# Kernel optimization log

Hardware: AMD Instinct MI355X
Metric: run time of the kernel (lower is better)

The kernel has to match this reference:

```python
import jax, jax.numpy as jnp
import numpy as np

B, S, N, E = 8, 32, 512, 8192
RC = DC = 64; SC = 256; EC = 512; P = 12


def setup_inputs() -> dict:
    key = jax.random.key(0)
    ks = jax.random.split(key, 20)
    def rn(k, shape, s=0.05):
        return jax.random.normal(k, shape, jnp.float32) * s
    return {
        "x": jax.random.normal(ks[0], (B, S, N), jnp.float32),
        "edge_index": jax.random.randint(ks[1], (2, E), 0, N),
        "edge_weight": jax.random.uniform(ks[2], (E,), jnp.float32),
        "start_w": rn(ks[3], (RC, 1)), "start_b": rn(ks[4], (RC,)),
        "filt_w": rn(ks[5], (DC, RC, 2)), "filt_b": rn(ks[6], (DC,)),
        "gate_w": rn(ks[7], (DC, RC, 2)), "gate_b": rn(ks[8], (DC,)),
        "gcn_w": rn(ks[9], (DC, DC)), "gcn_b": rn(ks[10], (DC,)),
        "res_w": rn(ks[11], (RC, DC)), "res_b": rn(ks[12], (RC,)),
        "skip_w": rn(ks[13], (SC, DC)), "skip_b": rn(ks[14], (SC,)),
        "end1_w": rn(ks[15], (EC, SC)), "end1_b": rn(ks[16], (EC,)),
        "end2_w": rn(ks[17], (P, EC)), "end2_b": rn(ks[18], (P,)),
    }


def _conv1x1(x, w, b):
    # Conv2d kernel (1,1): pure channel mix. x: [B,C,N,T], w: [O,C]
    return jnp.einsum('bcnt,oc->bont', x, w) + b[None, :, None, None]


def _conv_time2(x, w, b):
    return (jnp.einsum('bcnt,oc->bont', x[..., :-1], w[..., 0])
            + jnp.einsum('bcnt,oc->bont', x[..., 1:], w[..., 1])
            + b[None, :, None, None])


def _gcn_adj(edge_index, edge_weight, n):
    # PyG gcn_norm: add self-loops (weight 1), symmetric D^-1/2 (A+I) D^-1/2,
    # aggregation at edge_index[1] (target). Returns dense A_hat[tgt, src].
    ar = jnp.arange(n)
    row = jnp.concatenate([edge_index[0], ar])
    col = jnp.concatenate([edge_index[1], ar])
    w = jnp.concatenate([edge_weight, jnp.ones((n,), edge_weight.dtype)])
    deg = jnp.zeros((n,), w.dtype).at[col].add(w)
    dis = jnp.where(deg > 0, jax.lax.rsqrt(deg), jnp.zeros_like(deg))
    norm = dis[row] * w * dis[col]
    return jnp.zeros((n, n), w.dtype).at[col, row].add(norm)


def reference(x, edge_index, edge_weight, start_w, start_b, filt_w, filt_b,
              gate_w, gate_b, gcn_w, gcn_b, res_w, res_b, skip_w, skip_b,
              end1_w, end1_b, end2_w, end2_b):
    n = x.shape[2]
    A = _gcn_adj(edge_index, edge_weight, n)           # [N,N] sparse->dense (N small)
    h = jnp.transpose(x, (0, 2, 1))[:, None]           # [B,1,N,T]
    h = _conv1x1(h, start_w, start_b)                  # [B,RC,N,T]
    residual = h
    f = _conv_time2(h, filt_w, filt_b)                 # [B,DC,N,T-1]
    g = _conv_time2(h, gate_w, gate_b)
    # GCNConv applied to every (batch, time) slice == batched graph matmul
    fg = jnp.einsum('bcnt,oc->bont', f, gcn_w)         # x @ W^T
    fg = jnp.einsum('mn,bont->bomt', A, fg) + gcn_b[None, :, None, None]
    hg = jnp.tanh(fg) * jax.nn.sigmoid(g)              # gated activation
    skip = _conv1x1(hg, skip_w, skip_b)                # [B,SC,N,T-1]
    h = _conv1x1(hg, res_w, res_b) + residual[..., -hg.shape[3]:]
    out = jax.nn.relu(skip)
    out = jax.nn.relu(_conv1x1(out, end1_w, end1_b))
    out = _conv1x1(out, end2_w, end2_b)                # [B,P,N,T-1]
    # adaptive_avg_pool2d((N,1)) with H already N -> mean over time, squeeze
    return out.mean(axis=3)                            # [B,P,N]
```

## Files before the change

kernel.cpp:

```cpp
#include <hip/hip_runtime.h>

#define B_ 8
#define S_ 32
#define N_ 512
#define E_ 8192
#define T_ 31

typedef __attribute__((ext_vector_type(8))) __bf16 bf16x8;
typedef __attribute__((ext_vector_type(4))) float f32x4;
typedef unsigned short u16;
typedef unsigned int u32;

__device__ __forceinline__ u16 f2b(float f) {
    union { float f; u32 u; } v; v.f = f;
    u32 r = v.u + 0x7FFF + ((v.u >> 16) & 1);
    return (u16)(r >> 16);
}

__device__ __forceinline__ u32 cvtpk(float lo, float hi) {
    u32 r;
    asm("v_cvt_pk_bf16_f32 %0, %1, %2" : "=v"(r) : "v"(lo), "v"(hi));
    return r;
}

__device__ __forceinline__ f32x4 mfma16(bf16x8 a, bf16x8 b, f32x4 c) {
    return __builtin_amdgcn_mfma_f32_16x16x32_bf16(a, b, c, 0, 0, 0);
}

__global__ void deg_k(const int* __restrict__ ei, const float* __restrict__ ew,
                      float* __restrict__ deg) {
    int e = blockIdx.x * 256 + threadIdx.x;
    if (e >= E_ + N_) return;
    int col; float w;
    if (e < E_) { col = ei[E_ + e]; w = ew[e]; }
    else        { col = e - E_;     w = 1.f;  }
    atomicAdd(deg + col, w);
}

__global__ void dis_coef_k(const float* __restrict__ deg, float* __restrict__ dis,
                           const float* __restrict__ start_w, const float* __restrict__ start_b,
                           const float* __restrict__ filt_w, const float* __restrict__ filt_b,
                           const float* __restrict__ gate_w, const float* __restrict__ gate_b,
                           const float* __restrict__ gcn_w, float* __restrict__ coef,
                           const float* __restrict__ end2_b, float* __restrict__ out) {
    if (blockIdx.x >= 3) {
        int i = (blockIdx.x - 3) * 256 + threadIdx.x;
        out[i] = end2_b[(i >> 9) % 12];
        return;
    }
    if (blockIdx.x < 2) {
        int n = blockIdx.x * 256 + threadIdx.x;
        float d = deg[n];
        dis[n] = (d > 0.f) ? rsqrtf(d) : 0.f;
        return;
    }
    __shared__ float W[16384];
    __shared__ float sw[64], sb[64], A0[64], A1[64], C0[64];
    const int tid = threadIdx.x;
    if (tid < 64) { sw[tid] = start_w[tid]; sb[tid] = start_b[tid]; }
#pragma unroll
    for (int k = 0; k < 32; ++k) W[tid + k * 256] = filt_w[tid + k * 256];
#pragma unroll
    for (int k = 0; k < 32; ++k) W[8192 + tid + k * 256] = gate_w[tid + k * 256];
    __syncthreads();
    if (tid < 128) {
        const int o = tid & 63;
        const float* Wb = W + ((tid >= 64) ? 8192 : 0);
        float a0 = 0, a1 = 0, c = 0;
        for (int rr = 0; rr < 64; ++rr) {
            int r = (rr + o) & 63;
            float f0 = Wb[(o * 64 + r) * 2], f1 = Wb[(o * 64 + r) * 2 + 1];
            a0 += f0 * sw[r]; a1 += f1 * sw[r]; c += (f0 + f1) * sb[r];
        }
        if (tid < 64) { A0[o] = a0; A1[o] = a1; C0[o] = c + filt_b[o]; }
        else { coef[192 + o] = a0; coef[256 + o] = a1; coef[320 + o] = c + gate_b[o]; }
    }
    __syncthreads();
#pragma unroll
    for (int k = 0; k < 16; ++k) W[tid + k * 256] = gcn_w[tid + k * 256];
    __syncthreads();
    if (tid < 64) {
        const int o = tid;
        float u0 = 0, u1 = 0, u2 = 0;
        for (int dd = 0; dd < 64; ++dd) {
            int d = (dd + o) & 63;
            float g = W[o * 64 + d];
            u0 += g * A0[d]; u1 += g * A1[d]; u2 += g * C0[d];
        }
        coef[o] = u0; coef[64 + o] = u1; coef[128 + o] = u2;
    }
}

__global__ void scat_wconv_k(const int* __restrict__ ei, const float* __restrict__ ew,
                             const float* __restrict__ dis,
                             const float* __restrict__ skip_w, const float* __restrict__ end1_w,
                             const float* __restrict__ end2_w,
                             u16* __restrict__ W1, u16* __restrict__ W2, u16* __restrict__ W3,
                             float* __restrict__ S, float* __restrict__ rs) {
    const int bid = blockIdx.x;
    if (bid < 512) {
        int i = bid * 256 + threadIdx.x;
        {
            int m = i & 7, lane = (i >> 3) & 63, ii = (i >> 9) & 3;
            int kkI = (i >> 11) & 7, pw = (i >> 14) & 1, wid = (i >> 15) & 3;
            int er = wid * 128 + pw * 64 + ii * 16 + (lane & 15);
            int col = kkI * 32 + (lane >> 4) * 8 + m;
            W2[i] = f2b(end1_w[er * 256 + col]);
        }
        if (i < 16384) {
            int m = i & 7, lane = (i >> 3) & 63, ii = (i >> 9) & 3;
            int kkI = (i >> 11) & 1, wid = (i >> 12) & 3;
            int sr = wid * 64 + ii * 16 + (lane & 15);
            int col = kkI * 32 + (lane >> 4) * 8 + m;
            W1[i] = f2b(skip_w[sr * 64 + col]);
        }
        if (i < 8192) {
            int m = i & 7, lane = (i >> 3) & 63, c = (i >> 9) & 1;
            int pw = (i >> 10) & 1, wid = (i >> 11) & 3;
            int p = lane & 15;
            int k = wid * 128 + pw * 64 + c * 32 + (lane >> 4) * 8 + m;
            int e = (k & 0x1E0) | (((k >> 3) & 3) << 2) | (k & 3) | (((k >> 2) & 1) << 4);
            W3[i] = f2b((p < 12) ? end2_w[p * 512 + e] : 0.f);
        }
        return;
    }
    int e = (bid - 512) * 256 + threadIdx.x;
    if (e >= E_ + N_) return;
    int row, col; float w;
    if (e < E_) { row = ei[e]; col = ei[E_ + e]; w = ew[e]; }
    else        { row = col = e - E_;            w = 1.f;  }
    float nv = dis[row] * w * dis[col];
    atomicAdd(S + row * N_ + col, nv);
    atomicAdd(rs + col, nv);
}

__global__ void y_k(const float* __restrict__ x, const float* __restrict__ S,
                    float* __restrict__ Y0, float* __restrict__ Y1) {
    __shared__ float xs[4][256];
    const int tid = threadIdx.x;
    const int m = (blockIdx.x & 1) * 256 + tid;
    const int nh = (blockIdx.x >> 1) & 1;
    const int ns = nh * 256;
    const int bt0 = blockIdx.y * 4;
#pragma unroll
    for (int i = 0; i < 4; ++i) {
        int idx = tid + i * 256;
        xs[idx >> 8][idx & 255] = x[(bt0 + (idx >> 8)) * 512 + ns + (idx & 255)];
    }
    __syncthreads();
    float a0 = 0, a1 = 0, a2 = 0, a3 = 0;
#pragma unroll 8
    for (int n = 0; n < 256; ++n) {
        float sv = S[(ns + n) * 512 + m];
        a0 += xs[0][n] * sv; a1 += xs[1][n] * sv;
        a2 += xs[2][n] * sv; a3 += xs[3][n] * sv;
    }
    float* Yd = nh ? Y1 : Y0;
    Yd[(bt0 + 0) * 512 + m] = a0; Yd[(bt0 + 1) * 512 + m] = a1;
    Yd[(bt0 + 2) * 512 + m] = a2; Yd[(bt0 + 3) * 512 + m] = a3;
}

__launch_bounds__(256, 2)
__global__ void fused_k(const float* __restrict__ x, const float* __restrict__ Y0,
                        const float* __restrict__ Y1,
                        const float* __restrict__ rs, const float* __restrict__ coef,
                        const float* __restrict__ gcn_b, const float* __restrict__ skip_b,
                        const float* __restrict__ end1_b,
                        const u16* __restrict__ W1, const u16* __restrict__ W2,
                        const u16* __restrict__ W3, float* __restrict__ out) {
    __shared__ __align__(16) u16 HG[64 * 64];
    __shared__ __align__(16) u16 SK[64 * 256];
    __shared__ float xs0[64], xs1[64], ys0[64], ys1[64], rsl[64];
    __shared__ float cf[384], gb[64], bsk[256], be1[512];

    const int tid = threadIdx.x;
    const int wid = tid >> 6;
    const int lane = tid & 63;
    const int lr = lane & 15;
    const int lh = lane >> 4;

    const int bid = blockIdx.x;
    const int ntile = bid & 7;
    const int btix = bid >> 3;
    const int t = btix % 31;
    const int b = btix / 31;
    const int n0 = ntile * 64;
    const int bt = b * 32 + t;

    if (tid < 64) {
        xs0[tid] = x[bt * 512 + n0 + tid];
        xs1[tid] = x[(bt + 1) * 512 + n0 + tid];
        ys0[tid] = Y0[bt * 512 + n0 + tid] + Y1[bt * 512 + n0 + tid];
        ys1[tid] = Y0[(bt + 1) * 512 + n0 + tid] + Y1[(bt + 1) * 512 + n0 + tid];
        rsl[tid] = rs[n0 + tid];
        gb[tid]  = gcn_b[tid];
    }
    cf[tid] = coef[tid];
    if (tid < 128) cf[256 + tid] = coef[256 + tid];
    bsk[tid] = skip_b[tid];
    be1[tid] = end1_b[tid];
    be1[tid + 256] = end1_b[tid + 256];
    __syncthreads();

#pragma unroll
    for (int k = 0; k < 8; ++k) {
        const int v = tid + k * 256;
        const int pix = v >> 5;
        const int o0 = (v & 31) << 1;
        float hv[2];
#pragma unroll
        for (int q = 0; q < 2; ++q) {
            const int o = o0 + q;
            const float fgv = cf[o] * ys0[pix] + cf[64 + o] * ys1[pix]
                            + cf[128 + o] * rsl[pix] + gb[o];
            const float ggv = cf[192 + o] * xs0[pix] + cf[256 + o] * xs1[pix] + cf[320 + o];
            const float e2f = __expf(2.f * fgv);
            const float eg  = __expf(ggv);
            hv[q] = __fdividef((e2f - 1.f) * eg, (e2f + 1.f) * (1.f + eg));
        }
        *(u32*)(HG + (pix << 6) + (o0 ^ ((pix & 7) << 3))) = cvtpk(hv[0], hv[1]);
    }
    __syncthreads();

    {
        const u16* w1b = W1 + wid * 4096 + lane * 8;
        f32x4 acc[4][4];
#pragma unroll
        for (int i = 0; i < 4; ++i)
#pragma unroll
            for (int j = 0; j < 4; ++j) acc[i][j] = (f32x4){0.f, 0.f, 0.f, 0.f};
#pragma unroll
        for (int kkI = 0; kkI < 2; ++kkI) {
            const int kb = kkI * 32 + lh * 8;
            bf16x8 a[4], bv[4];
#pragma unroll
            for (int i = 0; i < 4; ++i) {
                a[i] = *(const bf16x8*)(w1b + kkI * 2048 + i * 512);
                const int pr = i * 16 + lr;
                bv[i] = *(const bf16x8*)(HG + (pr << 6) + (kb ^ ((pr & 7) << 3)));
            }
#pragma unroll
            for (int i = 0; i < 4; ++i)
#pragma unroll
                for (int j = 0; j < 4; ++j)
                    acc[i][j] = mfma16(a[i], bv[j], acc[i][j]);
        }
#pragma unroll
        for (int i = 0; i < 4; ++i) {
#pragma unroll
            for (int j = 0; j < 4; ++j) {
                const int pix = j * 16 + lr;
                const int xw = (pix & 7) << 3;
                const int s = wid * 64 + i * 16 + lh * 4;
                const u32 w0 = cvtpk(fmaxf(acc[i][j][0] + bsk[s + 0], 0.f),
                                     fmaxf(acc[i][j][1] + bsk[s + 1], 0.f));
                const u32 w1 = cvtpk(fmaxf(acc[i][j][2] + bsk[s + 2], 0.f),
                                     fmaxf(acc[i][j][3] + bsk[s + 3], 0.f));
                *(u32*)(SK + (pix << 8) + (s ^ xw)) = w0;
                *(u32*)(SK + (pix << 8) + ((s + 2) ^ xw)) = w1;
            }
        }
    }
    __syncthreads();

    {
        f32x4 acc_out[4];
#pragma unroll
        for (int j = 0; j < 4; ++j) acc_out[j] = (f32x4){0.f, 0.f, 0.f, 0.f};

#pragma unroll
        for (int pass = 0; pass < 2; ++pass) {
            const int ep = wid * 128 + pass * 64;
            const u16* w2b = W2 + (wid * 2 + pass) * 16384 + lane * 8;
            f32x4 acc[4][4];
#pragma unroll
            for (int i = 0; i < 4; ++i)
#pragma unroll
                for (int j = 0; j < 4; ++j) acc[i][j] = (f32x4){0.f, 0.f, 0.f, 0.f};
#pragma unroll
            for (int kkI = 0; kkI < 8; ++kkI) {
                const int kb = kkI * 32 + lh * 8;
                bf16x8 a[4], bv[4];
#pragma unroll
                for (int i = 0; i < 4; ++i)
                    a[i] = *(const bf16x8*)(w2b + kkI * 2048 + i * 512);
#pragma unroll
                for (int j = 0; j < 4; ++j) {
                    const int pr = j * 16 + lr;
                    bv[j] = *(const bf16x8*)(SK + (pr << 8) + (kb ^ ((pr & 7) << 3)));
                }
#pragma unroll
                for (int i = 0; i < 4; ++i)
#pragma unroll
                    for (int j = 0; j < 4; ++j)
                        acc[i][j] = mfma16(a[i], bv[j], acc[i][j]);
            }
            u32 pk[4][4][2];
#pragma unroll
            for (int i = 0; i < 4; ++i) {
#pragma unroll
                for (int j = 0; j < 4; ++j) {
                    const int eb = ep + i * 16 + lh * 4;
                    pk[i][j][0] = cvtpk(fmaxf(acc[i][j][0] + be1[eb + 0], 0.f),
                                        fmaxf(acc[i][j][1] + be1[eb + 1], 0.f));
                    pk[i][j][1] = cvtpk(fmaxf(acc[i][j][2] + be1[eb + 2], 0.f),
                                        fmaxf(acc[i][j][3] + be1[eb + 3], 0.f));
                }
            }
            bf16x8 bfr[2];
#pragma unroll
            for (int c = 0; c < 2; ++c)
                bfr[c] = *(const bf16x8*)(W3 + (wid * 2 + pass) * 1024 + c * 512 + lane * 8);
#pragma unroll
            for (int j = 0; j < 4; ++j) {
#pragma unroll
                for (int c = 0; c < 2; ++c) {
                    union { u32 w[4]; bf16x8 v; } af;
                    af.w[0] = pk[2 * c][j][0];
                    af.w[1] = pk[2 * c][j][1];
                    af.w[2] = pk[2 * c + 1][j][0];
                    af.w[3] = pk[2 * c + 1][j][1];
                    acc_out[j] = mfma16(af.v, bfr[c], acc_out[j]);
                }
            }
        }
        __syncthreads();

        float* SKf = (float*)SK;
#pragma unroll
        for (int j = 0; j < 4; ++j)
#pragma unroll
            for (int r = 0; r < 4; ++r)
                SKf[wid * 1024 + (j * 16 + lh * 4 + r) * 16 + lr] = acc_out[j][r];
    }
    __syncthreads();

    {
        const f32x4* Sv = (const f32x4*)SK;
        f32x4 sum = Sv[tid] + Sv[256 + tid] + Sv[512 + tid] + Sv[768 + tid];
        const int pix = tid >> 2;
        const int p0 = (tid & 3) << 2;
        if (p0 < 12) {
#pragma unroll
            for (int r = 0; r < 4; ++r)
                atomicAdd(out + (b * 12 + p0 + r) * 512 + n0 + pix, sum[r] * (1.f / 31.f));
        }
    }
}

extern "C" void kernel_launch(void* const* d_in, const int* in_sizes, int n_in,
                              void* d_out, int out_size, void* d_ws, size_t ws_size,
                              hipStream_t stream) {
    const float* x       = (const float*)d_in[0];
    const int*   ei      = (const int*)  d_in[1];
    const float* ew      = (const float*)d_in[2];
    const float* start_w = (const float*)d_in[3];
    const float* start_b = (const float*)d_in[4];
    const float* filt_w  = (const float*)d_in[5];
    const float* filt_b  = (const float*)d_in[6];
    const float* gate_w  = (const float*)d_in[7];
    const float* gate_b  = (const float*)d_in[8];
    const float* gcn_w   = (const float*)d_in[9];
    const float* gcn_b   = (const float*)d_in[10];
    const float* skip_w  = (const float*)d_in[13];
    const float* skip_b  = (const float*)d_in[14];
    const float* end1_w  = (const float*)d_in[15];
    const float* end1_b  = (const float*)d_in[16];
    const float* end2_w  = (const float*)d_in[17];
    const float* end2_b  = (const float*)d_in[18];
    float* out = (float*)d_out;

    char* ws = (char*)d_ws;
    float* S    = (float*)(ws);
    float* deg  = (float*)(ws + 1048576);
    float* rs   = (float*)(ws + 1050624);
    float* dis  = (float*)(ws + 1052672);
    float* Y0   = (float*)(ws + 1054720);
    float* coef = (float*)(ws + 1579008);
    u16*   W1   = (u16*)  (ws + 1580544);
    u16*   W2   = (u16*)  (ws + 1613312);
    u16*   W3   = (u16*)  (ws + 1875456);
    float* Y1   = (float*)(ws + 1891840);

    hipMemsetAsync(S, 0, 1048576 + 4096, stream);
    hipLaunchKernelGGL(deg_k,      dim3(34),  dim3(256), 0, stream, ei, ew, deg);
    hipLaunchKernelGGL(dis_coef_k, dim3(195), dim3(256), 0, stream, deg, dis,
                       start_w, start_b, filt_w, filt_b, gate_w, gate_b, gcn_w, coef,
                       end2_b, out);
    hipLaunchKernelGGL(scat_wconv_k, dim3(546), dim3(256), 0, stream, ei, ew, dis,
                       skip_w, end1_w, end2_w, W1, W2, W3, S, rs);
    hipLaunchKernelGGL(y_k,    dim3(4, 64), dim3(256), 0, stream, x, S, Y0, Y1);
    hipLaunchKernelGGL(fused_k, dim3(1984), dim3(256), 0, stream,
                       x, Y0, Y1, rs, coef, gcn_b, skip_b, end1_b, W1, W2, W3, out);
}
```

Baseline: 101.0 us.

## Split small reductions across more threads, widen y_k split-K, prefetch MFMA weights

The coefficient-precompute loops in dis_coef_k are now spread over all 256 threads, with partial sums combined through shared memory, where before only 64 or 128 threads did the work. y_k splits its reduction over N into four partial buffers instead of two and launches twice as many blocks, and fused_k sums the four partials. In fused_k the W1 fragments are loaded before the prologue, W2 fragments are double-buffered one k-step ahead, and W3 loads are hoisted ahead of the main loop. These changes target serial tails and global-load latency, at the cost of more registers, extra Y traffic and an added barrier.

```diff
diff --git a/kernel.cpp b/kernel.cpp
--- a/kernel.cpp
+++ b/kernel.cpp
@@ -56,6 +56,8 @@
     }
     __shared__ float W[16384];
     __shared__ float sw[64], sb[64], A0[64], A1[64], C0[64];
+    __shared__ float r0[128][2], r1[128][2], r2[128][2];
+    __shared__ float u0s[64][4], u1s[64][4], u2s[64][4];
     const int tid = threadIdx.x;
     if (tid < 64) { sw[tid] = start_w[tid]; sb[tid] = start_b[tid]; }
 #pragma unroll
@@ -63,15 +65,24 @@
 #pragma unroll
     for (int k = 0; k < 32; ++k) W[8192 + tid + k * 256] = gate_w[tid + k * 256];
     __syncthreads();
+    {
+        const int task = tid >> 1, half = tid & 1;
+        const int o = task & 63;
+        const float* Wb = W + ((task >= 64) ? 8192 : 0);
+        float a0 = 0, a1 = 0, c = 0;
+        for (int rr = 0; rr < 32; ++rr) {
+            int r = (half * 32 + rr + o) & 63;
+            float f0 = Wb[(o * 64 + r) * 2], f1 = Wb[(o * 64 + r) * 2 + 1];
+            a0 += f0 * sw[r]; a1 += f1 * sw[r]; c += (f0 + f1) * sb[r];
+        }
+        r0[task][half] = a0; r1[task][half] = a1; r2[task][half] = c;
+    }
+    __syncthreads();
     if (tid < 128) {
         const int o = tid & 63;
-        const float* Wb = W + ((tid >= 64) ? 8192 : 0);
-        float a0 = 0, a1 = 0, c = 0;
-        for (int rr = 0; rr < 64; ++rr) {
-            int r = (rr + o) & 63;
-            float f0 = Wb[(o * 64 + r) * 2], f1 = Wb[(o * 64 + r) * 2 + 1];
-            a0 += f0 * sw[r]; a1 += f1 * sw[r]; c += (f0 + f1) * sb[r];
-        }
+        float a0 = r0[tid][0] + r0[tid][1];
+        float a1 = r1[tid][0] + r1[tid][1];
+        float c  = r2[tid][0] + r2[tid][1];
         if (tid < 64) { A0[o] = a0; A1[o] = a1; C0[o] = c + filt_b[o]; }
         else { coef[192 + o] = a0; coef[256 + o] = a1; coef[320 + o] = c + gate_b[o]; }
     }
@@ -79,15 +90,22 @@
 #pragma unroll
     for (int k = 0; k < 16; ++k) W[tid + k * 256] = gcn_w[tid + k * 256];
     __syncthreads();
+    {
+        const int o = tid & 63, q = tid >> 6;
+        float u0 = 0, u1 = 0, u2 = 0;
+        for (int dd = 0; dd < 16; ++dd) {
+            int d = q * 16 + ((dd + o) & 15);
+            float g = W[o * 64 + d];
+            u0 += g * A0[d]; u1 += g * A1[d]; u2 += g * C0[d];
+        }
+        u0s[o][q] = u0; u1s[o][q] = u1; u2s[o][q] = u2;
+    }
+    __syncthreads();
     if (tid < 64) {
         const int o = tid;
-        float u0 = 0, u1 = 0, u2 = 0;
-        for (int dd = 0; dd < 64; ++dd) {
-            int d = (dd + o) & 63;
-            float g = W[o * 64 + d];
-            u0 += g * A0[d]; u1 += g * A1[d]; u2 += g * C0[d];
-        }
-        coef[o] = u0; coef[64 + o] = u1; coef[128 + o] = u2;
+        coef[o]       = u0s[o][0] + u0s[o][1] + u0s[o][2] + u0s[o][3];
+        coef[64 + o]  = u1s[o][0] + u1s[o][1] + u1s[o][2] + u1s[o][3];
+        coef[128 + o] = u2s[o][0] + u2s[o][1] + u2s[o][2] + u2s[o][3];
     }
 }
 
@@ -135,34 +153,33 @@
 }
 
 __global__ void y_k(const float* __restrict__ x, const float* __restrict__ S,
-                    float* __restrict__ Y0, float* __restrict__ Y1) {
-    __shared__ float xs[4][256];
+                    float* __restrict__ Y) {
+    __shared__ float xs[4][128];
     const int tid = threadIdx.x;
     const int m = (blockIdx.x & 1) * 256 + tid;
-    const int nh = (blockIdx.x >> 1) & 1;
-    const int ns = nh * 256;
+    const int q = blockIdx.x >> 1;
+    const int ns = q * 128;
     const int bt0 = blockIdx.y * 4;
 #pragma unroll
-    for (int i = 0; i < 4; ++i) {
+    for (int i = 0; i < 2; ++i) {
         int idx = tid + i * 256;
-        xs[idx >> 8][idx & 255] = x[(bt0 + (idx >> 8)) * 512 + ns + (idx & 255)];
+        xs[idx >> 7][idx & 127] = x[(bt0 + (idx >> 7)) * 512 + ns + (idx & 127)];
     }
     __syncthreads();
     float a0 = 0, a1 = 0, a2 = 0, a3 = 0;
 #pragma unroll 8
-    for (int n = 0; n < 256; ++n) {
+    for (int n = 0; n < 128; ++n) {
         float sv = S[(ns + n) * 512 + m];
         a0 += xs[0][n] * sv; a1 += xs[1][n] * sv;
         a2 += xs[2][n] * sv; a3 += xs[3][n] * sv;
     }
-    float* Yd = nh ? Y1 : Y0;
+    float* Yd = Y + q * 131072;
     Yd[(bt0 + 0) * 512 + m] = a0; Yd[(bt0 + 1) * 512 + m] = a1;
     Yd[(bt0 + 2) * 512 + m] = a2; Yd[(bt0 + 3) * 512 + m] = a3;
 }
 
 __launch_bounds__(256, 2)
-__global__ void fused_k(const float* __restrict__ x, const float* __restrict__ Y0,
-                        const float* __restrict__ Y1,
+__global__ void fused_k(const float* __restrict__ x, const float* __restrict__ Y,
                         const float* __restrict__ rs, const float* __restrict__ coef,
                         const float* __restrict__ gcn_b, const float* __restrict__ skip_b,
                         const float* __restrict__ end1_b,
@@ -187,11 +204,22 @@
     const int n0 = ntile * 64;
     const int bt = b * 32 + t;
 
+    bf16x8 a1f[2][4];
+    {
+        const u16* w1b = W1 + wid * 4096 + lane * 8;
+#pragma unroll
+        for (int kkI = 0; kkI < 2; ++kkI)
+#pragma unroll
+            for (int i = 0; i < 4; ++i)
+                a1f[kkI][i] = *(const bf16x8*)(w1b + kkI * 2048 + i * 512);
+    }
+
     if (tid < 64) {
-        xs0[tid] = x[bt * 512 + n0 + tid];
-        xs1[tid] = x[(bt + 1) * 512 + n0 + tid];
-        ys0[tid] = Y0[bt * 512 + n0 + tid] + Y1[bt * 512 + n0 + tid];
-        ys1[tid] = Y0[(bt + 1) * 512 + n0 + tid] + Y1[(bt + 1) * 512 + n0 + tid];
+        const int a0 = bt * 512 + n0 + tid, a1 = (bt + 1) * 512 + n0 + tid;
+        xs0[tid] = x[a0];
+        xs1[tid] = x[a1];
+        ys0[tid] = Y[a0] + Y[131072 + a0] + Y[262144 + a0] + Y[393216 + a0];
+        ys1[tid] = Y[a1] + Y[131072 + a1] + Y[262144 + a1] + Y[393216 + a1];
         rsl[tid] = rs[n0 + tid];
         gb[tid]  = gcn_b[tid];
     }
@@ -223,7 +251,6 @@
     __syncthreads();
 
     {
-        const u16* w1b = W1 + wid * 4096 + lane * 8;
         f32x4 acc[4][4];
 #pragma unroll
         for (int i = 0; i < 4; ++i)
@@ -232,18 +259,17 @@
 #pragma unroll
         for (int kkI = 0; kkI < 2; ++kkI) {
             const int kb = kkI * 32 + lh * 8;
-            bf16x8 a[4], bv[4];
-#pragma unroll
-            for (int i = 0; i < 4; ++i) {
-                a[i] = *(const bf16x8*)(w1b + kkI * 2048 + i * 512);
-                const int pr = i * 16 + lr;
-                bv[i] = *(const bf16x8*)(HG + (pr << 6) + (kb ^ ((pr & 7) << 3)));
+            bf16x8 bv[4];
+#pragma unroll
+            for (int j = 0; j < 4; ++j) {
+                const int pr = j * 16 + lr;
+                bv[j] = *(const bf16x8*)(HG + (pr << 6) + (kb ^ ((pr & 7) << 3)));
             }
 #pragma unroll
             for (int i = 0; i < 4; ++i)
 #pragma unroll
                 for (int j = 0; j < 4; ++j)
-                    acc[i][j] = mfma16(a[i], bv[j], acc[i][j]);
+                    acc[i][j] = mfma16(a1f[kkI][i], bv[j], acc[i][j]);
         }
 #pragma unroll
         for (int i = 0; i < 4; ++i) {
@@ -272,18 +298,29 @@
         for (int pass = 0; pass < 2; ++pass) {
             const int ep = wid * 128 + pass * 64;
             const u16* w2b = W2 + (wid * 2 + pass) * 16384 + lane * 8;
+            bf16x8 bfr[2];
+#pragma unroll
+            for (int c = 0; c < 2; ++c)
+                bfr[c] = *(const bf16x8*)(W3 + (wid * 2 + pass) * 1024 + c * 512 + lane * 8);
             f32x4 acc[4][4];
 #pragma unroll
             for (int i = 0; i < 4; ++i)
 #pragma unroll
                 for (int j = 0; j < 4; ++j) acc[i][j] = (f32x4){0.f, 0.f, 0.f, 0.f};
+            bf16x8 aC[4];
+#pragma unroll
+            for (int i = 0; i < 4; ++i)
+                aC[i] = *(const bf16x8*)(w2b + i * 512);
 #pragma unroll
             for (int kkI = 0; kkI < 8; ++kkI) {
+                bf16x8 aN[4];
+                if (kkI < 7) {
+#pragma unroll
+                    for (int i = 0; i < 4; ++i)
+                        aN[i] = *(const bf16x8*)(w2b + (kkI + 1) * 2048 + i * 512);
+                }
                 const int kb = kkI * 32 + lh * 8;
-                bf16x8 a[4], bv[4];
-#pragma unroll
-                for (int i = 0; i < 4; ++i)
-                    a[i] = *(const bf16x8*)(w2b + kkI * 2048 + i * 512);
+                bf16x8 bv[4];
 #pragma unroll
                 for (int j = 0; j < 4; ++j) {
                     const int pr = j * 16 + lr;
@@ -293,7 +330,11 @@
                 for (int i = 0; i < 4; ++i)
 #pragma unroll
                     for (int j = 0; j < 4; ++j)
-                        acc[i][j] = mfma16(a[i], bv[j], acc[i][j]);
+                        acc[i][j] = mfma16(aC[i], bv[j], acc[i][j]);
+                if (kkI < 7) {
+#pragma unroll
+                    for (int i = 0; i < 4; ++i) aC[i] = aN[i];
+                }
             }
             u32 pk[4][4][2];
 #pragma unroll
@@ -307,10 +348,6 @@
                                         fmaxf(acc[i][j][3] + be1[eb + 3], 0.f));
                 }
             }
-            bf16x8 bfr[2];
-#pragma unroll
-            for (int c = 0; c < 2; ++c)
-                bfr[c] = *(const bf16x8*)(W3 + (wid * 2 + pass) * 1024 + c * 512 + lane * 8);
 #pragma unroll
             for (int j = 0; j < 4; ++j) {
 #pragma unroll
@@ -375,12 +412,11 @@
     float* deg  = (float*)(ws + 1048576);
     float* rs   = (float*)(ws + 1050624);
     float* dis  = (float*)(ws + 1052672);
-    float* Y0   = (float*)(ws + 1054720);
     float* coef = (float*)(ws + 1579008);
     u16*   W1   = (u16*)  (ws + 1580544);
     u16*   W2   = (u16*)  (ws + 1613312);
     u16*   W3   = (u16*)  (ws + 1875456);
-    float* Y1   = (float*)(ws + 1891840);
+    float* Y    = (float*)(ws + 1891840);
 
     hipMemsetAsync(S, 0, 1048576 + 4096, stream);
     hipLaunchKernelGGL(deg_k,      dim3(34),  dim3(256), 0, stream, ei, ew, deg);
@@ -389,7 +425,7 @@
                        end2_b, out);
     hipLaunchKernelGGL(scat_wconv_k, dim3(546), dim3(256), 0, stream, ei, ew, dis,
                        skip_w, end1_w, end2_w, W1, W2, W3, S, rs);
-    hipLaunchKernelGGL(y_k,    dim3(4, 64), dim3(256), 0, stream, x, S, Y0, Y1);
+    hipLaunchKernelGGL(y_k,    dim3(8, 64), dim3(256), 0, stream, x, S, Y);
     hipLaunchKernelGGL(fused_k, dim3(1984), dim3(256), 0, stream,
-                       x, Y0, Y1, rs, coef, gcn_b, skip_b, end1_b, W1, W2, W3, out);
-}
+                       x, Y, rs, coef, gcn_b, skip_b, end1_b, W1, W2, W3, out);
+}
```

Measured after the change: 83.11 us. -17.7%, faster.
